# Performance work log

Hardware: AMD Instinct MI355X
Metric: run time of the kernel (lower is better)

The kernel has to match this reference:

```python
import jax, jax.numpy as jnp
import numpy as np

B, S, D, H = 4, 1024, 1024, 16
HS = D // H  # head_size = 64


def setup_inputs() -> dict:
    key = jax.random.key(0)
    ks = jax.random.split(key, 6)
    scale = 1.0 / np.sqrt(D)
    data = jax.random.normal(ks[0], (B, S, D), dtype=jnp.float32)
    # Per-head projection weights, stacked: [H, D, HS] (no bias, per nn.Linear(bias=False))
    Wq = jax.random.normal(ks[1], (H, D, HS), dtype=jnp.float32) * scale
    Wk = jax.random.normal(ks[2], (H, D, HS), dtype=jnp.float32) * scale
    Wv = jax.random.normal(ks[3], (H, D, HS), dtype=jnp.float32) * scale
    # Output projection: [H*HS, D] plus bias [D]
    Wo = jax.random.normal(ks[4], (H * HS, D), dtype=jnp.float32) * scale
    bo = jax.random.normal(ks[5], (D,), dtype=jnp.float32) * 0.01
    return {"data": data, "Wq": Wq, "Wk": Wk, "Wv": Wv, "Wo": Wo, "bo": bo}


def reference(data, Wq, Wk, Wv, Wo, bo):
    b, s, d = data.shape
    # Per-head Q/K/V projections (self-attention: encoder_data = data)
    q = jnp.einsum('bsd,hde->bhse', data, Wq)  # [B,H,S,HS]
    k = jnp.einsum('bsd,hde->bhse', data, Wk)
    v = jnp.einsum('bsd,hde->bhse', data, Wv)
    # NOTE: original scales by sqrt(embedding_dimension), not sqrt(head_size)
    scores = jnp.einsum('bhse,bhte->bhst', q, k) / jnp.sqrt(jnp.asarray(d, dtype=data.dtype))
    # causal mask (tril of block_size, sliced to [S, S])
    causal = jnp.tril(jnp.ones((s, s), dtype=bool))
    scores = jnp.where(causal, scores, -jnp.inf)
    attn = jax.nn.softmax(scores, axis=-1)  # dropout rate 0.0 -> identity
    out = jnp.einsum('bhst,bhte->bhse', attn, v)  # [B,H,S,HS]
    # concat heads along feature dim (head order matches ModuleList order)
    out = out.transpose(0, 2, 1, 3).reshape(b, s, -1)  # [B,S,H*HS]
    return out @ Wo + bo
```

## Files before the change

kernel.cpp:

```cpp
#include <hip/hip_runtime.h>
#include <hip/hip_bf16.h>
#include <stdint.h>

#define NEG_SENTINEL (-1e30f)

typedef short s16x8 __attribute__((ext_vector_type(8)));
typedef float f32x4 __attribute__((ext_vector_type(4)));

__device__ __forceinline__ ushort f2bf(float f) {
  union { float f; uint32_t u; } v; v.f = f;
  uint32_t u = v.u;
  u += 0x7fffu + ((u >> 16) & 1u);
  return (ushort)(u >> 16);
}
__device__ __forceinline__ ushort f2bf_rn(float f) {
  union { float f; uint32_t u; } v; v.f = f;
  return (ushort)((v.u + 0x8000u) >> 16);
}

__device__ __forceinline__ void async_ld16(ushort* lds, const ushort* g) {
  __builtin_amdgcn_global_load_lds(
      (const __attribute__((address_space(1))) uint32_t*)g,
      (__attribute__((address_space(3))) uint32_t*)lds, 16, 0, 0);
}

__global__ __launch_bounds__(256) void convert_f32_bf16(
    const float* __restrict__ src, ushort* __restrict__ dst) {
  long i = ((long)blockIdx.x * 256 + threadIdx.x) * 8;
  float4 a = *(const float4*)(src + i);
  float4 b = *(const float4*)(src + i + 4);
  union { ushort u[8]; uint4 v; } o;
  o.u[0] = f2bf(a.x); o.u[1] = f2bf(a.y); o.u[2] = f2bf(a.z); o.u[3] = f2bf(a.w);
  o.u[4] = f2bf(b.x); o.u[5] = f2bf(b.y); o.u[6] = f2bf(b.z); o.u[7] = f2bf(b.w);
  *(uint4*)(dst + i) = o.v;
}

__global__ __launch_bounds__(256) void transpose_w3(
    const float* __restrict__ Wq, const float* __restrict__ Wk,
    const float* __restrict__ Wv, ushort* __restrict__ WTall) {
  const int z = blockIdx.z;
  const int matsel = z >> 4;
  const float* src = (matsel == 0 ? Wq : (matsel == 1 ? Wk : Wv)) +
                     (long)(z & 15) * 65536;
  ushort* dst = WTall + (long)z * 65536;
  const int it = blockIdx.y;
  __shared__ __align__(16) ushort tile[64 * 72];
  const int tid = threadIdx.x;
#pragma unroll
  for (int p = 0; p < 4; ++p) {
    int chunk = tid + p * 256;
    int r = chunk >> 4, c0 = (chunk & 15) * 4;
    float4 f = *(const float4*)(src + (long)(it * 64 + r) * 64 + c0);
    union { ushort u[4]; uint2 v; } o;
    o.u[0] = f2bf(f.x); o.u[1] = f2bf(f.y); o.u[2] = f2bf(f.z); o.u[3] = f2bf(f.w);
    *(uint2*)&tile[r * 72 + c0] = o.v;
  }
  __syncthreads();
#pragma unroll
  for (int p = 0; p < 2; ++p) {
    int chunk = tid + p * 256;
    int r = chunk >> 3, c0 = (chunk & 7) * 8;
    union { ushort u[8]; uint4 v; } tmp;
#pragma unroll
    for (int k2 = 0; k2 < 8; ++k2) tmp.u[k2] = tile[(c0 + k2) * 72 + r];
    *(uint4*)(dst + (long)r * 1024 + it * 64 + c0) = tmp.v;
  }
}

__global__ __launch_bounds__(256) void transpose_cvt(
    const float* __restrict__ src, ushort* __restrict__ dst) {
  const int jt = blockIdx.x;
  const int it = blockIdx.y;
  __shared__ __align__(16) ushort tile[64 * 72];
  const int tid = threadIdx.x;
#pragma unroll
  for (int p = 0; p < 4; ++p) {
    int chunk = tid + p * 256;
    int r = chunk >> 4, c0 = (chunk & 15) * 4;
    float4 f = *(const float4*)(src + (long)(it * 64 + r) * 1024 + jt * 64 + c0);
    union { ushort u[4]; uint2 v; } o;
    o.u[0] = f2bf(f.x); o.u[1] = f2bf(f.y); o.u[2] = f2bf(f.z); o.u[3] = f2bf(f.w);
    *(uint2*)&tile[r * 72 + c0] = o.v;
  }
  __syncthreads();
#pragma unroll
  for (int p = 0; p < 2; ++p) {
    int chunk = tid + p * 256;
    int r = chunk >> 3, c0 = (chunk & 7) * 8;
    union { ushort u[8]; uint4 v; } tmp;
#pragma unroll
    for (int k2 = 0; k2 < 8; ++k2) tmp.u[k2] = tile[(c0 + k2) * 72 + r];
    *(uint4*)(dst + (long)(jt * 64 + r) * 1024 + it * 64 + c0) = tmp.v;
  }
}

__device__ __forceinline__ void gemm_core_128x128(
    const ushort* __restrict__ A, const ushort* __restrict__ BT,
    ushort* As, ushort* Bs, f32x4 acc[4][4]) {
  const int tid = threadIdx.x;
  const int lane = tid & 63, w = tid >> 6, quad = lane >> 4, l15 = lane & 15;
  const int wm = w >> 1, wn = w & 1;
  for (int k0 = 0; k0 < 1024; k0 += 64) {
#pragma unroll
    for (int p = 0; p < 4; ++p) {
      int c = tid + p * 256;
      int r = c >> 3, c8 = (c & 7) * 8;
      async_ld16(As + c * 8, A + (long)r * 1024 + k0 + c8);
      async_ld16(Bs + c * 8, BT + (long)r * 1024 + k0 + c8);
    }
    __syncthreads();
#pragma unroll
    for (int kk = 0; kk < 64; kk += 32) {
      s16x8 af[4], bfr[4];
#pragma unroll
      for (int mi = 0; mi < 4; ++mi)
        af[mi] = *(const s16x8*)&As[(wm * 64 + mi * 16 + l15) * 64 + kk + quad * 8];
#pragma unroll
      for (int ni = 0; ni < 4; ++ni)
        bfr[ni] = *(const s16x8*)&Bs[(wn * 64 + ni * 16 + l15) * 64 + kk + quad * 8];
#pragma unroll
      for (int mi = 0; mi < 4; ++mi)
#pragma unroll
        for (int ni = 0; ni < 4; ++ni)
          acc[mi][ni] = __builtin_amdgcn_mfma_f32_16x16x32_bf16(
              af[mi], bfr[ni], acc[mi][ni], 0, 0, 0);
    }
    __syncthreads();
  }
}

__global__ __launch_bounds__(256) void qkv_proj(
    const ushort* __restrict__ dataB, const ushort* __restrict__ WTall,
    ushort* __restrict__ QKV) {
  __shared__ __align__(16) ushort smem[128 * 136];
  ushort* As = smem;
  ushort* Bs = smem + 8192;
  ushort* Ct = smem;
  const int m0 = blockIdx.x * 128;
  const int n0 = blockIdx.y * 128;
  f32x4 acc[4][4];
  const f32x4 z = {0.f, 0.f, 0.f, 0.f};
#pragma unroll
  for (int mi = 0; mi < 4; ++mi)
#pragma unroll
    for (int ni = 0; ni < 4; ++ni) acc[mi][ni] = z;
  gemm_core_128x128(dataB + (long)m0 * 1024, WTall + (long)n0 * 1024, As, Bs, acc);

  const int tid = threadIdx.x;
  const int lane = tid & 63, w = tid >> 6, quad = lane >> 4, l15 = lane & 15;
  const int wm = w >> 1, wn = w & 1;
  const int matsel = n0 >> 10;
  const int bI = m0 >> 10, s0 = m0 & 1023;

  if (matsel < 2) {
    const float sc = (matsel == 0) ? 0.03125f : 1.0f;
    ushort* base = QKV + (long)matsel * 4194304 + (long)bI * 1048576;
#pragma unroll
    for (int mi = 0; mi < 4; ++mi) {
#pragma unroll
      for (int ni = 0; ni < 4; ++ni) {
        int n = n0 + wn * 64 + ni * 16 + l15;
        int h = (n >> 6) & 15, e = n & 63;
        ushort* col = base + (long)h * 65536 + e;
#pragma unroll
        for (int i = 0; i < 4; ++i) {
          int s = s0 + wm * 64 + mi * 16 + quad * 4 + i;
          col[s * 64] = f2bf(acc[mi][ni][i] * sc);
        }
      }
    }
  } else {
#pragma unroll
    for (int mi = 0; mi < 4; ++mi)
#pragma unroll
      for (int ni = 0; ni < 4; ++ni)
#pragma unroll
        for (int i = 0; i < 4; ++i)
          Ct[(wn * 64 + ni * 16 + l15) * 136 + wm * 64 + mi * 16 + quad * 4 + i] =
              f2bf(acc[mi][ni][i]);
    __syncthreads();
    ushort* base = QKV + 8388608 + (long)bI * 1048576;
#pragma unroll
    for (int p = 0; p < 8; ++p) {
      int c = tid + p * 256;
      int r = c >> 4, m8 = (c & 15) * 8;
      int h = ((n0 + r) >> 6) & 15, e = (n0 + r) & 63;
      *(uint4*)(base + (long)h * 65536 + e * 1024 + s0 + m8) =
          *(const uint4*)&Ct[r * 136 + m8];
    }
  }
}

__global__ __launch_bounds__(256) void out_proj(
    const ushort* __restrict__ Ocat, const ushort* __restrict__ WoT,
    const float* __restrict__ bo, float* __restrict__ out) {
  __shared__ __align__(16) ushort As[128 * 64];
  __shared__ __align__(16) ushort Bs[128 * 64];
  const int m0 = blockIdx.x * 128;
  const int n0 = blockIdx.y * 128;
  f32x4 acc[4][4];
  const f32x4 z = {0.f, 0.f, 0.f, 0.f};
#pragma unroll
  for (int mi = 0; mi < 4; ++mi)
#pragma unroll
    for (int ni = 0; ni < 4; ++ni) acc[mi][ni] = z;
  gemm_core_128x128(Ocat + (long)m0 * 1024, WoT + (long)n0 * 1024, As, Bs, acc);

  const int tid = threadIdx.x;
  const int lane = tid & 63, w = tid >> 6, quad = lane >> 4, l15 = lane & 15;
  const int wm = w >> 1, wn = w & 1;
#pragma unroll
  for (int mi = 0; mi < 4; ++mi) {
#pragma unroll
    for (int ni = 0; ni < 4; ++ni) {
#pragma unroll
      for (int i = 0; i < 4; ++i) {
        int m = m0 + wm * 64 + mi * 16 + quad * 4 + i;
        int n = n0 + wn * 64 + ni * 16 + l15;
        out[(long)m * 1024 + n] = acc[mi][ni][i] + bo[n];
      }
    }
  }
}

__global__ __launch_bounds__(512, 4) void attn_kernel(
    const ushort* __restrict__ QKV, ushort* __restrict__ Ocat) {
  __shared__ __align__(16) ushort Ks[128 * 72];
  __shared__ __align__(16) ushort Vs[64 * 136];
  __shared__ __align__(16) ushort Ps[8 * 16 * 136];
  const int qt = 7 - blockIdx.y;
  const int bh = blockIdx.x;
  const int b = bh >> 4, h = bh & 15;
  const int tid = threadIdx.x;
  const int w = tid >> 6, lane = tid & 63, quad = lane >> 4, l15 = lane & 15;
  const int q0 = qt * 128;

  const ushort* Qp = QKV + (long)bh * 65536;
  const ushort* Kp = QKV + 4194304 + (long)bh * 65536;
  const ushort* VTp = QKV + 8388608 + (long)bh * 65536;

  const int qrow = q0 + w * 16 + l15;
  s16x8 qf0 = *(const s16x8*)(Qp + (long)qrow * 64 + quad * 8);
  s16x8 qf1 = *(const s16x8*)(Qp + (long)qrow * 64 + 32 + quad * 8);

  f32x4 oacc[4];
  const f32x4 z = {0.f, 0.f, 0.f, 0.f};
#pragma unroll
  for (int et = 0; et < 4; ++et) oacc[et] = z;
  float l_i[4] = {0.f, 0.f, 0.f, 0.f};

  ushort* Psw = Ps + w * (16 * 136);
  const int nj = qt + 1;

  for (int j = 0; j < nj; ++j) {
#pragma unroll
    for (int p = 0; p < 2; ++p) {
      int c = tid + p * 512;
      { int r = c >> 3, c8 = (c & 7) * 8;
        *(uint4*)&Ks[r * 72 + c8] = *(const uint4*)(Kp + (long)(j * 128 + r) * 64 + c8); }
      { int r = c >> 4, c8 = (c & 15) * 8;
        *(uint4*)&Vs[r * 136 + c8] = *(const uint4*)(VTp + (long)r * 1024 + j * 128 + c8); }
    }
    __syncthreads();

    f32x4 sacc[8];
#pragma unroll
    for (int nt = 0; nt < 8; ++nt) sacc[nt] = z;
#pragma unroll
    for (int kk = 0; kk < 64; kk += 32) {
      s16x8 a = kk ? qf1 : qf0;
#pragma unroll
      for (int nt = 0; nt < 8; ++nt) {
        s16x8 bfr = *(const s16x8*)&Ks[(nt * 16 + l15) * 72 + kk + quad * 8];
        sacc[nt] = __builtin_amdgcn_mfma_f32_16x16x32_bf16(a, bfr, sacc[nt], 0, 0, 0);
      }
    }

    if (j == qt) {
      const int srow = q0 + w * 16 + quad * 4;
#pragma unroll
      for (int nt = 0; nt < 8; ++nt) {
#pragma unroll
        for (int i = 0; i < 4; ++i) {
          int tg = j * 128 + nt * 16 + l15;
          if (tg > srow + i) sacc[nt][i] = NEG_SENTINEL;
        }
      }
    }

#pragma unroll
    for (int i = 0; i < 4; ++i) {
#pragma unroll
      for (int nt = 0; nt < 8; ++nt) {
        float p = __expf(sacc[nt][i]);
        Psw[(quad * 4 + i) * 136 + nt * 16 + l15] = f2bf_rn(p);
        l_i[i] += p;
      }
    }

#pragma unroll
    for (int kk = 0; kk < 128; kk += 32) {
      s16x8 pa = *(const s16x8*)&Psw[l15 * 136 + kk + quad * 8];
#pragma unroll
      for (int et = 0; et < 4; ++et) {
        s16x8 vb = *(const s16x8*)&Vs[(et * 16 + l15) * 136 + kk + quad * 8];
        oacc[et] = __builtin_amdgcn_mfma_f32_16x16x32_bf16(pa, vb, oacc[et], 0, 0, 0);
      }
    }
    __syncthreads();
  }

#pragma unroll
  for (int i = 0; i < 4; ++i) {
#pragma unroll
    for (int d = 1; d < 16; d <<= 1) l_i[i] += __shfl_xor(l_i[i], d, 64);
  }

  ushort* Ob = Ocat + ((long)(b * 1024 + q0 + w * 16) * 1024) + h * 64;
#pragma unroll
  for (int et = 0; et < 4; ++et) {
#pragma unroll
    for (int i = 0; i < 4; ++i) {
      float denom = l_i[i];
      float v = oacc[et][i] / (denom > 0.f ? denom : 1.0f);
      Ob[(long)(quad * 4 + i) * 1024 + et * 16 + l15] = f2bf_rn(v);
    }
  }
}

extern "C" void kernel_launch(void* const* d_in, const int* in_sizes, int n_in,
                              void* d_out, int out_size, void* d_ws, size_t ws_size,
                              hipStream_t stream) {
  const float* data = (const float*)d_in[0];
  const float* Wq = (const float*)d_in[1];
  const float* Wk = (const float*)d_in[2];
  const float* Wv = (const float*)d_in[3];
  const float* Wo = (const float*)d_in[4];
  const float* bo = (const float*)d_in[5];
  float* out = (float*)d_out;

  ushort* ws = (ushort*)d_ws;
  ushort* QKV = ws;
  ushort* dataB = ws + 12582912;
  ushort* Ocat = ws + 16777216;
  ushort* WTall = ws + 20971520;
  ushort* WoT = ws + 20971520 + 3145728;

  dim3 blk(256);
  convert_f32_bf16<<<dim3(2048), blk, 0, stream>>>(data, dataB);
  transpose_w3<<<dim3(1, 16, 48), blk, 0, stream>>>(Wq, Wk, Wv, WTall);
  transpose_cvt<<<dim3(16, 16), blk, 0, stream>>>(Wo, WoT);
  qkv_proj<<<dim3(32, 24), blk, 0, stream>>>(dataB, WTall, QKV);
  attn_kernel<<<dim3(64, 8), dim3(512), 0, stream>>>(QKV, Ocat);
  out_proj<<<dim3(32, 8), blk, 0, stream>>>(Ocat, WoT, bo, out);
}
```

Baseline: 185.1 us.

## Merge prep kernels into one launch and use async LDS loads in attention

The three preprocessing kernels (data conversion, QKV weight transpose, Wo transpose) become a single launch whose work is chosen by block index range. This removes two kernel launches and their gaps. Separately, the attention kernel now loads K and V tiles with direct global-to-LDS async loads into unpadded shared buffers instead of going through registers. Dropping the padding may add LDS bank conflicts on the MFMA operand reads, since row strides become 128 and 256 bytes.

```diff
diff --git a/kernel.cpp b/kernel.cpp
--- a/kernel.cpp
+++ b/kernel.cpp
@@ -24,33 +24,46 @@
       (__attribute__((address_space(3))) uint32_t*)lds, 16, 0, 0);
 }
 
-__global__ __launch_bounds__(256) void convert_f32_bf16(
-    const float* __restrict__ src, ushort* __restrict__ dst) {
-  long i = ((long)blockIdx.x * 256 + threadIdx.x) * 8;
-  float4 a = *(const float4*)(src + i);
-  float4 b = *(const float4*)(src + i + 4);
-  union { ushort u[8]; uint4 v; } o;
-  o.u[0] = f2bf(a.x); o.u[1] = f2bf(a.y); o.u[2] = f2bf(a.z); o.u[3] = f2bf(a.w);
-  o.u[4] = f2bf(b.x); o.u[5] = f2bf(b.y); o.u[6] = f2bf(b.z); o.u[7] = f2bf(b.w);
-  *(uint4*)(dst + i) = o.v;
-}
-
-__global__ __launch_bounds__(256) void transpose_w3(
-    const float* __restrict__ Wq, const float* __restrict__ Wk,
-    const float* __restrict__ Wv, ushort* __restrict__ WTall) {
-  const int z = blockIdx.z;
-  const int matsel = z >> 4;
-  const float* src = (matsel == 0 ? Wq : (matsel == 1 ? Wk : Wv)) +
-                     (long)(z & 15) * 65536;
-  ushort* dst = WTall + (long)z * 65536;
-  const int it = blockIdx.y;
+__global__ __launch_bounds__(256) void prep_kernel(
+    const float* __restrict__ data, const float* __restrict__ Wq,
+    const float* __restrict__ Wk, const float* __restrict__ Wv,
+    const float* __restrict__ Wo, ushort* __restrict__ dataB,
+    ushort* __restrict__ WTall, ushort* __restrict__ WoT) {
+  const int blk = blockIdx.x;
+  const int tid = threadIdx.x;
+  if (blk < 2048) {
+    long i = ((long)blk * 256 + tid) * 8;
+    float4 a = *(const float4*)(data + i);
+    float4 b = *(const float4*)(data + i + 4);
+    union { ushort u[8]; uint4 v; } o;
+    o.u[0] = f2bf(a.x); o.u[1] = f2bf(a.y); o.u[2] = f2bf(a.z); o.u[3] = f2bf(a.w);
+    o.u[4] = f2bf(b.x); o.u[5] = f2bf(b.y); o.u[6] = f2bf(b.z); o.u[7] = f2bf(b.w);
+    *(uint4*)(dataB + i) = o.v;
+    return;
+  }
   __shared__ __align__(16) ushort tile[64 * 72];
-  const int tid = threadIdx.x;
+  const float* src;
+  ushort* dst;
+  int srcCols, dstRowStride, it, jt;
+  if (blk < 2816) {
+    int t = blk - 2048;
+    int z = t >> 4;
+    it = t & 15;  jt = 0;
+    int matsel = z >> 4;
+    src = (matsel == 0 ? Wq : (matsel == 1 ? Wk : Wv)) + (long)(z & 15) * 65536;
+    dst = WTall + (long)z * 65536;
+    srcCols = 64; dstRowStride = 1024;
+  } else {
+    int t = blk - 2816;
+    jt = t & 15; it = t >> 4;
+    src = Wo; dst = WoT;
+    srcCols = 1024; dstRowStride = 1024;
+  }
 #pragma unroll
   for (int p = 0; p < 4; ++p) {
     int chunk = tid + p * 256;
     int r = chunk >> 4, c0 = (chunk & 15) * 4;
-    float4 f = *(const float4*)(src + (long)(it * 64 + r) * 64 + c0);
+    float4 f = *(const float4*)(src + (long)(it * 64 + r) * srcCols + jt * 64 + c0);
     union { ushort u[4]; uint2 v; } o;
     o.u[0] = f2bf(f.x); o.u[1] = f2bf(f.y); o.u[2] = f2bf(f.z); o.u[3] = f2bf(f.w);
     *(uint2*)&tile[r * 72 + c0] = o.v;
@@ -63,34 +76,7 @@
     union { ushort u[8]; uint4 v; } tmp;
 #pragma unroll
     for (int k2 = 0; k2 < 8; ++k2) tmp.u[k2] = tile[(c0 + k2) * 72 + r];
-    *(uint4*)(dst + (long)r * 1024 + it * 64 + c0) = tmp.v;
-  }
-}
-
-__global__ __launch_bounds__(256) void transpose_cvt(
-    const float* __restrict__ src, ushort* __restrict__ dst) {
-  const int jt = blockIdx.x;
-  const int it = blockIdx.y;
-  __shared__ __align__(16) ushort tile[64 * 72];
-  const int tid = threadIdx.x;
-#pragma unroll
-  for (int p = 0; p < 4; ++p) {
-    int chunk = tid + p * 256;
-    int r = chunk >> 4, c0 = (chunk & 15) * 4;
-    float4 f = *(const float4*)(src + (long)(it * 64 + r) * 1024 + jt * 64 + c0);
-    union { ushort u[4]; uint2 v; } o;
-    o.u[0] = f2bf(f.x); o.u[1] = f2bf(f.y); o.u[2] = f2bf(f.z); o.u[3] = f2bf(f.w);
-    *(uint2*)&tile[r * 72 + c0] = o.v;
-  }
-  __syncthreads();
-#pragma unroll
-  for (int p = 0; p < 2; ++p) {
-    int chunk = tid + p * 256;
-    int r = chunk >> 3, c0 = (chunk & 7) * 8;
-    union { ushort u[8]; uint4 v; } tmp;
-#pragma unroll
-    for (int k2 = 0; k2 < 8; ++k2) tmp.u[k2] = tile[(c0 + k2) * 72 + r];
-    *(uint4*)(dst + (long)(jt * 64 + r) * 1024 + it * 64 + c0) = tmp.v;
+    *(uint4*)(dst + (long)(jt * 64 + r) * dstRowStride + it * 64 + c0) = tmp.v;
   }
 }
 
@@ -225,8 +211,8 @@
 
 __global__ __launch_bounds__(512, 4) void attn_kernel(
     const ushort* __restrict__ QKV, ushort* __restrict__ Ocat) {
-  __shared__ __align__(16) ushort Ks[128 * 72];
-  __shared__ __align__(16) ushort Vs[64 * 136];
+  __shared__ __align__(16) ushort Ks[128 * 64];
+  __shared__ __align__(16) ushort Vs[64 * 128];
   __shared__ __align__(16) ushort Ps[8 * 16 * 136];
   const int qt = 7 - blockIdx.y;
   const int bh = blockIdx.x;
@@ -256,10 +242,9 @@
 #pragma unroll
     for (int p = 0; p < 2; ++p) {
       int c = tid + p * 512;
-      { int r = c >> 3, c8 = (c & 7) * 8;
-        *(uint4*)&Ks[r * 72 + c8] = *(const uint4*)(Kp + (long)(j * 128 + r) * 64 + c8); }
-      { int r = c >> 4, c8 = (c & 15) * 8;
-        *(uint4*)&Vs[r * 136 + c8] = *(const uint4*)(VTp + (long)r * 1024 + j * 128 + c8); }
+      async_ld16(Ks + c * 8, Kp + (long)j * 8192 + c * 8);
+      int r = c >> 4, c8 = (c & 15) * 8;
+      async_ld16(Vs + c * 8, VTp + (long)r * 1024 + j * 128 + c8);
     }
     __syncthreads();
 
@@ -271,7 +256,7 @@
       s16x8 a = kk ? qf1 : qf0;
 #pragma unroll
       for (int nt = 0; nt < 8; ++nt) {
-        s16x8 bfr = *(const s16x8*)&Ks[(nt * 16 + l15) * 72 + kk + quad * 8];
+        s16x8 bfr = *(const s16x8*)&Ks[(nt * 16 + l15) * 64 + kk + quad * 8];
         sacc[nt] = __builtin_amdgcn_mfma_f32_16x16x32_bf16(a, bfr, sacc[nt], 0, 0, 0);
       }
     }
@@ -303,7 +288,7 @@
       s16x8 pa = *(const s16x8*)&Psw[l15 * 136 + kk + quad * 8];
 #pragma unroll
       for (int et = 0; et < 4; ++et) {
-        s16x8 vb = *(const s16x8*)&Vs[(et * 16 + l15) * 136 + kk + quad * 8];
+        s16x8 vb = *(const s16x8*)&Vs[(et * 16 + l15) * 128 + kk + quad * 8];
         oacc[et] = __builtin_amdgcn_mfma_f32_16x16x32_bf16(pa, vb, oacc[et], 0, 0, 0);
       }
     }
@@ -347,9 +332,8 @@
   ushort* WoT = ws + 20971520 + 3145728;
 
   dim3 blk(256);
-  convert_f32_bf16<<<dim3(2048), blk, 0, stream>>>(data, dataB);
-  transpose_w3<<<dim3(1, 16, 48), blk, 0, stream>>>(Wq, Wk, Wv, WTall);
-  transpose_cvt<<<dim3(16, 16), blk, 0, stream>>>(Wo, WoT);
+  prep_kernel<<<dim3(3072), blk, 0, stream>>>(data, Wq, Wk, Wv, Wo,
+                                              dataB, WTall, WoT);
   qkv_proj<<<dim3(32, 24), blk, 0, stream>>>(dataB, WTall, QKV);
   attn_kernel<<<dim3(64, 8), dim3(512), 0, stream>>>(QKV, Ocat);
   out_proj<<<dim3(32, 8), blk, 0, stream>>>(Ocat, WoT, bo, out);
```

Result: slower. 203.7 us (+10.1%).
